# Optimization experiments

Measured on AMD Instinct MI355X. Metric: run time of the kernel, lower is better.

The kernel has to match this reference:

```python
import jax, jax.numpy as jnp
import numpy as np

T, IN, OUT = 16384, 4096, 4096


def setup_inputs() -> dict:
    key = jax.random.key(0)
    k1, k2, k3, k4, k5 = jax.random.split(key, 5)
    x = jax.random.randint(k1, (T, IN), -128, 128, dtype=jnp.int32)      # int8-valued activations
    weight = jax.random.randint(k2, (OUT, IN), -128, 128, dtype=jnp.int32)  # int8-valued weights
    bias = jax.random.randint(k3, (OUT,), -128, 128, dtype=jnp.int32)    # int8-valued bias
    # requant scales: alpha = a_scale*w_scale/o_scale, beta = b_scale/o_scale
    alpha = jax.random.uniform(k4, (1,), jnp.float32, 1e-4, 1e-3)
    beta = jax.random.uniform(k5, (1,), jnp.float32, 0.5, 1.5)
    return {"x": x, "weight": weight, "bias": bias, "alpha": alpha, "beta": beta}


def reference(x, weight, bias, alpha, beta):
    # INT8 GEMM with int32 accumulation: acc[t,o] = sum_i x[t,i] * W[o,i]
    acc = jnp.einsum('ti,oi->to', x, weight,
                     preferred_element_type=jnp.int32)  # [T, OUT] int32
    # inline dequant + bias + requant epilogue
    y = acc.astype(jnp.float32) * alpha + bias.astype(jnp.float32) * beta
    # round and saturate to int8 output (W8A8B8O8)
    out = jnp.clip(jnp.round(y), -128.0, 127.0).astype(jnp.int8)
    return out
```

## Files before the change

kernel.cpp:

```cpp
#include <hip/hip_runtime.h>
#include <stdint.h>

constexpr int T_DIM   = 16384;
constexpr int IN_DIM  = 4096;
constexpr int OUT_DIM = 4096;

using int32x4 = __attribute__((ext_vector_type(4))) int;

#define GLOAD_LDS16(g, l)                                                     \
    __builtin_amdgcn_global_load_lds(                                         \
        (const __attribute__((address_space(1))) void*)(uintptr_t)(g),        \
        (__attribute__((address_space(3))) void*)(uintptr_t)(l), 16, 0, 0)

__global__ void pack_swz(const int* __restrict__ src, int8_t* __restrict__ dst,
                         int rows, int cols) {
    int64_t tid = (int64_t)blockIdx.x * blockDim.x + threadIdx.x;
    int64_t nchunks = (int64_t)rows * (cols / 16);
    if (tid >= nchunks) return;
    int row  = (int)(tid / (cols / 16));
    int cidx = (int)(tid % (cols / 16));
    const int32x4* s4 =
        reinterpret_cast<const int32x4*>(src + (int64_t)row * cols + (cidx << 4));
    uint32_t p[4];
#pragma unroll
    for (int v = 0; v < 4; ++v) {
        int32x4 t = s4[v];
        p[v] = (uint32_t)(t[0] & 0xff) | ((uint32_t)(t[1] & 0xff) << 8) |
               ((uint32_t)(t[2] & 0xff) << 16) | ((uint32_t)(t[3] & 0xff) << 24);
    }
    int cs = (cidx & ~3) | ((cidx & 3) ^ ((row >> 1) & 3));
    *reinterpret_cast<int32x4*>(dst + (int64_t)row * cols + (cs << 4)) =
        *reinterpret_cast<int32x4*>(p);
}

constexpr int BM = 256, BN = 256, BK = 64;
constexpr int NT    = IN_DIM / BK;
constexpr int ATILE = BM * BK;
constexpr int BUFSZ = 2 * ATILE;

__global__ __launch_bounds__(512, 2)
void gemm_i8_8p(const int8_t* __restrict__ x8, const int8_t* __restrict__ w8,
                const int* __restrict__ bias, const float* __restrict__ alphap,
                const float* __restrict__ betap, int* __restrict__ out) {
    __shared__ __align__(16) int8_t lds[4 * BUFSZ];

    const int tid  = threadIdx.x;
    const int lane = tid & 63;
    const int wid  = tid >> 6;
    const int wr   = wid >> 2;
    const int wc   = wid & 3;

    const int nwg = gridDim.x;
    const int cpx = nwg >> 3;
    const int bid = blockIdx.x;
    const int swz = (bid & 7) * cpx + (bid >> 3);
    const int bm  = swz >> 4;
    const int bn  = swz & 15;
    const int brow = bm * BM;
    const int bcol = bn * BN;

    const float alpha = *alphap;
    const float beta  = *betap;

    const int g = lane >> 4;
    const int r = lane & 15;

    auto stageA = [&](int kt, int8_t* buf) {
#pragma unroll
        for (int l = 0; l < 2; ++l) {
            const int off = l * 8192 + tid * 16;
            const int row = off >> 6;
            GLOAD_LDS16(x8 + (int64_t)(brow + row) * IN_DIM + kt * BK + (off & 63),
                        buf + off);
        }
    };
    auto stageB = [&](int kt, int8_t* buf) {
#pragma unroll
        for (int l = 0; l < 2; ++l) {
            const int off = l * 8192 + tid * 16;
            const int row = off >> 6;
            GLOAD_LDS16(w8 + (int64_t)(bcol + row) * IN_DIM + kt * BK + (off & 63),
                        buf + ATILE + off);
        }
    };
    auto ldA = [&](const int8_t* Ab, int m) -> int32x4 {
        const int row = wr * 128 + m * 16 + r;
        const int sc  = g ^ ((row >> 1) & 3);
        return *reinterpret_cast<const int32x4*>(Ab + row * BK + (sc << 4));
    };
    auto ldB = [&](const int8_t* Bb, int n) -> int32x4 {
        const int row = wc * 64 + n * 16 + r;
        const int sc  = g ^ ((row >> 1) & 3);
        return *reinterpret_cast<const int32x4*>(Bb + row * BK + (sc << 4));
    };

    int32x4 acc[8][4] = {};

#define KTILE(T, BIDX, PF, VM)                                                 \
    do {                                                                       \
        const int8_t* Ab = lds + (BIDX) * BUFSZ;                               \
        const int8_t* Bb = Ab + ATILE;                                         \
        int8_t* nxt = lds + (((BIDX) + 3) & 3) * BUFSZ;                        \
        int32x4 bf[4], af[4];                                                  \
        _Pragma("unroll") for (int n = 0; n < 4; ++n) bf[n] = ldB(Bb, n);      \
        _Pragma("unroll") for (int m = 0; m < 4; ++m) af[m] = ldA(Ab, m);      \
        if (PF) stageA((T) + 3, nxt);                                          \
        __builtin_amdgcn_s_barrier();                                          \
        asm volatile("s_waitcnt lgkmcnt(0)");                                  \
        __builtin_amdgcn_s_setprio(1);                                         \
        _Pragma("unroll") for (int m = 0; m < 4; ++m)                          \
            _Pragma("unroll") for (int n = 0; n < 4; ++n)                      \
                acc[m][n] = __builtin_amdgcn_mfma_i32_16x16x64_i8(             \
                    af[m], bf[n], acc[m][n], 0, 0, 0);                         \
        __builtin_amdgcn_s_setprio(0);                                         \
        __builtin_amdgcn_s_barrier();                                          \
        _Pragma("unroll") for (int m = 0; m < 4; ++m) af[m] = ldA(Ab, 4 + m);  \
        if (PF) stageB((T) + 3, nxt);                                          \
        __builtin_amdgcn_s_barrier();                                          \
        asm volatile("s_waitcnt lgkmcnt(0)");                                  \
        __builtin_amdgcn_s_setprio(1);                                         \
        _Pragma("unroll") for (int m = 0; m < 4; ++m)                          \
            _Pragma("unroll") for (int n = 0; n < 4; ++n)                      \
                acc[4 + m][n] = __builtin_amdgcn_mfma_i32_16x16x64_i8(         \
                    af[m], bf[n], acc[4 + m][n], 0, 0, 0);                     \
        __builtin_amdgcn_s_setprio(0);                                         \
        if ((VM) == 8)      asm volatile("s_waitcnt vmcnt(8)" ::: "memory");   \
        else if ((VM) == 4) asm volatile("s_waitcnt vmcnt(4)" ::: "memory");   \
        else if ((VM) == 0) asm volatile("s_waitcnt vmcnt(0)" ::: "memory");   \
        __builtin_amdgcn_s_barrier();                                          \
        asm volatile("" ::: "memory");     \
    } while (0)

    stageA(0, lds);            stageB(0, lds);
    stageA(1, lds + BUFSZ);    stageB(1, lds + BUFSZ);
    stageA(2, lds + 2*BUFSZ);  stageB(2, lds + 2*BUFSZ);
    asm volatile("s_waitcnt vmcnt(8)" ::: "memory");
    __builtin_amdgcn_s_barrier();
    asm volatile("" ::: "memory");

#pragma unroll 1
    for (int tt = 0; tt < NT - 4; tt += 4) {
        KTILE(tt + 0, 0, true, 8);
        KTILE(tt + 1, 1, true, 8);
        KTILE(tt + 2, 2, true, 8);
        KTILE(tt + 3, 3, true, 8);
    }
    KTILE(NT - 4, 0, true,  8);
    KTILE(NT - 3, 1, false, 4);
    KTILE(NT - 2, 2, false, 0);
    KTILE(NT - 1, 3, false, -1);
#undef KTILE

    const int r4 = (lane >> 4) * 4;
    const int cl = lane & 15;
#pragma unroll
    for (int n = 0; n < 4; ++n) {
        const int col = bcol + wc * 64 + n * 16 + cl;
        const float bterm = (float)bias[col] * beta;
#pragma unroll
        for (int m = 0; m < 8; ++m) {
            const int row0 = brow + wr * 128 + m * 16 + r4;
#pragma unroll
            for (int j = 0; j < 4; ++j) {
                float y = (float)acc[m][n][j] * alpha + bterm;
                y = rintf(y);
                y = fminf(fmaxf(y, -128.0f), 127.0f);
                out[(int64_t)(row0 + j) * OUT_DIM + col] = (int)y;
            }
        }
    }
}

__global__ __launch_bounds__(256)
void gemm_i8_fb(const int* __restrict__ x32, const int* __restrict__ w32,
                const int* __restrict__ bias, const float* __restrict__ alphap,
                const float* __restrict__ betap, int* __restrict__ out) {
    constexpr int FBM = 128, FBK = 128;
    __shared__ int8_t lA[FBM * FBK];
    __shared__ int8_t lB[FBM * FBK];

    const int tid  = threadIdx.x;
    const int wid  = tid >> 6;
    const int lane = tid & 63;
    const int nwg = gridDim.x;
    const int cpx = nwg >> 3;
    const int bid = blockIdx.x;
    const int swz = (bid & 7) * cpx + (bid >> 3);
    const int brow = (swz >> 5) * FBM;
    const int bcol = (swz & 31) * FBM;
    const int wr = wid >> 1, wc = wid & 1;
    const float alpha = *alphap;
    const float beta  = *betap;

    int32x4 acc[4][4] = {};
    for (int kt = 0; kt < IN_DIM / FBK; ++kt) {
        const int64_t kbase = (int64_t)kt * FBK;
#pragma unroll
        for (int q = 0; q < 4; ++q) {
            const int off = wid * 4096 + q * 1024 + lane * 16;
            const int row = off >> 7;
            const int k   = off & 127;
            const int* ga = x32 + (int64_t)(brow + row) * IN_DIM + kbase + k;
            const int* gb = w32 + (int64_t)(bcol + row) * IN_DIM + kbase + k;
            uint32_t pa[4], pb[4];
#pragma unroll
            for (int v = 0; v < 4; ++v) {
                int32x4 ta = reinterpret_cast<const int32x4*>(ga)[v];
                int32x4 tb = reinterpret_cast<const int32x4*>(gb)[v];
                pa[v] = (uint32_t)(ta[0] & 0xff) | ((uint32_t)(ta[1] & 0xff) << 8) |
                        ((uint32_t)(ta[2] & 0xff) << 16) | ((uint32_t)(ta[3] & 0xff) << 24);
                pb[v] = (uint32_t)(tb[0] & 0xff) | ((uint32_t)(tb[1] & 0xff) << 8) |
                        ((uint32_t)(tb[2] & 0xff) << 16) | ((uint32_t)(tb[3] & 0xff) << 24);
            }
            const int sc = ((k >> 4) ^ (row & 7)) << 4;
            *reinterpret_cast<int32x4*>(lA + row * FBK + sc) = *reinterpret_cast<int32x4*>(pa);
            *reinterpret_cast<int32x4*>(lB + row * FBK + sc) = *reinterpret_cast<int32x4*>(pb);
        }
        __syncthreads();
#pragma unroll
        for (int ks = 0; ks < 2; ++ks) {
            const int gg = lane >> 4, rr = lane & 15;
            const int lc = ks * 4 + gg;
            int32x4 af[4], bf[4];
#pragma unroll
            for (int m = 0; m < 4; ++m) {
                const int row = wr * 64 + m * 16 + rr;
                af[m] = *reinterpret_cast<const int32x4*>(lA + row * FBK + ((lc ^ (row & 7)) << 4));
            }
#pragma unroll
            for (int n = 0; n < 4; ++n) {
                const int row = wc * 64 + n * 16 + rr;
                bf[n] = *reinterpret_cast<const int32x4*>(lB + row * FBK + ((lc ^ (row & 7)) << 4));
            }
#pragma unroll
            for (int m = 0; m < 4; ++m)
#pragma unroll
                for (int n = 0; n < 4; ++n)
                    acc[m][n] = __builtin_amdgcn_mfma_i32_16x16x64_i8(af[m], bf[n], acc[m][n], 0, 0, 0);
        }
        __syncthreads();
    }
    const int r4 = (lane >> 4) * 4;
    const int cl = lane & 15;
#pragma unroll
    for (int n = 0; n < 4; ++n) {
        const int col = bcol + wc * 64 + n * 16 + cl;
        const float bterm = (float)bias[col] * beta;
#pragma unroll
        for (int m = 0; m < 4; ++m) {
            const int row0 = brow + wr * 64 + m * 16 + r4;
#pragma unroll
            for (int j = 0; j < 4; ++j) {
                float y = (float)acc[m][n][j] * alpha + bterm;
                y = rintf(y);
                y = fminf(fmaxf(y, -128.0f), 127.0f);
                out[(int64_t)(row0 + j) * OUT_DIM + col] = (int)y;
            }
        }
    }
}

extern "C" void kernel_launch(void* const* d_in, const int* in_sizes, int n_in,
                              void* d_out, int out_size, void* d_ws, size_t ws_size,
                              hipStream_t stream) {
    const int*   x     = (const int*)d_in[0];
    const int*   w     = (const int*)d_in[1];
    const int*   bias  = (const int*)d_in[2];
    const float* alpha = (const float*)d_in[3];
    const float* beta  = (const float*)d_in[4];
    int*         out   = (int*)d_out;

    const size_t need = (size_t)T_DIM * IN_DIM + (size_t)OUT_DIM * IN_DIM;

    if (ws_size >= need) {
        int8_t* x8 = (int8_t*)d_ws;
        int8_t* w8 = x8 + (size_t)T_DIM * IN_DIM;
        {
            int64_t nch = (int64_t)T_DIM * (IN_DIM / 16);
            pack_swz<<<(int)((nch + 255) / 256), 256, 0, stream>>>(x, x8, T_DIM, IN_DIM);
        }
        {
            int64_t nch = (int64_t)OUT_DIM * (IN_DIM / 16);
            pack_swz<<<(int)((nch + 255) / 256), 256, 0, stream>>>(w, w8, OUT_DIM, IN_DIM);
        }
        const int grid = (T_DIM / BM) * (OUT_DIM / BN);
        gemm_i8_8p<<<grid, 512, 0, stream>>>(x8, w8, bias, alpha, beta, out);
    } else {
        const int grid = (T_DIM / 128) * (OUT_DIM / 128);
        gemm_i8_fb<<<grid, 256, 0, stream>>>(x, w, bias, alpha, beta, out);
    }
}
```

Measured before the change: 395.7 us.

## Collapse K-tile into single MFMA phase with precomputed LDS and global offsets

Restructures each K-tile step so all four global-to-LDS prefetches for the next stage are issued up front. All 8 A and 4 B fragments are then read from LDS and all 32 MFMAs run in one block, replacing the earlier two-phase split that needed three barriers per tile. Global pointers advance by BK each tile and LDS fragment offsets are precomputed once, which cuts per-tile address arithmetic. This is meant to reduce barrier and sync overhead, but holding all 8 A fragments raises VGPR pressure and removes the interleaving of LDS reads with MFMA.

After: 394.6 us. Within noise of the previous version (-0.3%).

```diff
diff --git a/kernel.cpp b/kernel.cpp
--- a/kernel.cpp
+++ b/kernel.cpp
@@ -65,90 +65,80 @@
     const int g = lane >> 4;
     const int r = lane & 15;
 
-    auto stageA = [&](int kt, int8_t* buf) {
-#pragma unroll
-        for (int l = 0; l < 2; ++l) {
-            const int off = l * 8192 + tid * 16;
-            const int row = off >> 6;
-            GLOAD_LDS16(x8 + (int64_t)(brow + row) * IN_DIM + kt * BK + (off & 63),
-                        buf + off);
-        }
-    };
-    auto stageB = [&](int kt, int8_t* buf) {
-#pragma unroll
-        for (int l = 0; l < 2; ++l) {
-            const int off = l * 8192 + tid * 16;
-            const int row = off >> 6;
-            GLOAD_LDS16(w8 + (int64_t)(bcol + row) * IN_DIM + kt * BK + (off & 63),
-                        buf + ATILE + off);
-        }
-    };
-    auto ldA = [&](const int8_t* Ab, int m) -> int32x4 {
+    const int offL0 = tid * 16;
+    const int offL1 = 8192 + tid * 16;
+    const int rowL0 = offL0 >> 6, inL0 = offL0 & 63;
+    const int rowL1 = offL1 >> 6, inL1 = offL1 & 63;
+    const int8_t* pA0 = x8 + (int64_t)(brow + rowL0) * IN_DIM + inL0;
+    const int8_t* pA1 = x8 + (int64_t)(brow + rowL1) * IN_DIM + inL1;
+    const int8_t* pB0 = w8 + (int64_t)(bcol + rowL0) * IN_DIM + inL0;
+    const int8_t* pB1 = w8 + (int64_t)(bcol + rowL1) * IN_DIM + inL1;
+    const int dA0 = offL0, dA1 = offL1;
+    const int dB0 = ATILE + offL0, dB1 = ATILE + offL1;
+
+    int aoff[8], boff[4];
+#pragma unroll
+    for (int m = 0; m < 8; ++m) {
         const int row = wr * 128 + m * 16 + r;
-        const int sc  = g ^ ((row >> 1) & 3);
-        return *reinterpret_cast<const int32x4*>(Ab + row * BK + (sc << 4));
-    };
-    auto ldB = [&](const int8_t* Bb, int n) -> int32x4 {
+        aoff[m] = row * BK + ((g ^ ((row >> 1) & 3)) << 4);
+    }
+#pragma unroll
+    for (int n = 0; n < 4; ++n) {
         const int row = wc * 64 + n * 16 + r;
-        const int sc  = g ^ ((row >> 1) & 3);
-        return *reinterpret_cast<const int32x4*>(Bb + row * BK + (sc << 4));
-    };
+        boff[n] = ATILE + row * BK + ((g ^ ((row >> 1) & 3)) << 4);
+    }
 
     int32x4 acc[8][4] = {};
 
-#define KTILE(T, BIDX, PF, VM)                                                 \
+#define KTILE(BIDX, PF, VM)                                                    \
     do {                                                                       \
-        const int8_t* Ab = lds + (BIDX) * BUFSZ;                               \
-        const int8_t* Bb = Ab + ATILE;                                         \
+        const int8_t* buf = lds + (BIDX) * BUFSZ;                              \
         int8_t* nxt = lds + (((BIDX) + 3) & 3) * BUFSZ;                        \
-        int32x4 bf[4], af[4];                                                  \
-        _Pragma("unroll") for (int n = 0; n < 4; ++n) bf[n] = ldB(Bb, n);      \
-        _Pragma("unroll") for (int m = 0; m < 4; ++m) af[m] = ldA(Ab, m);      \
-        if (PF) stageA((T) + 3, nxt);                                          \
-        __builtin_amdgcn_s_barrier();                                          \
-        asm volatile("s_waitcnt lgkmcnt(0)");                                  \
+        if (PF) {                                                              \
+            GLOAD_LDS16(pA0, nxt + dA0);  GLOAD_LDS16(pA1, nxt + dA1);         \
+            GLOAD_LDS16(pB0, nxt + dB0);  GLOAD_LDS16(pB1, nxt + dB1);         \
+            pA0 += BK; pA1 += BK; pB0 += BK; pB1 += BK;                        \
+        }                                                                      \
+        int32x4 af[8], bf[4];                                                  \
+        _Pragma("unroll") for (int n = 0; n < 4; ++n)                          \
+            bf[n] = *reinterpret_cast<const int32x4*>(buf + boff[n]);          \
+        _Pragma("unroll") for (int m = 0; m < 8; ++m)                          \
+            af[m] = *reinterpret_cast<const int32x4*>(buf + aoff[m]);          \
         __builtin_amdgcn_s_setprio(1);                                         \
-        _Pragma("unroll") for (int m = 0; m < 4; ++m)                          \
+        _Pragma("unroll") for (int m = 0; m < 8; ++m)                          \
             _Pragma("unroll") for (int n = 0; n < 4; ++n)                      \
                 acc[m][n] = __builtin_amdgcn_mfma_i32_16x16x64_i8(             \
                     af[m], bf[n], acc[m][n], 0, 0, 0);                         \
-        __builtin_amdgcn_s_setprio(0);                                         \
-        __builtin_amdgcn_s_barrier();                                          \
-        _Pragma("unroll") for (int m = 0; m < 4; ++m) af[m] = ldA(Ab, 4 + m);  \
-        if (PF) stageB((T) + 3, nxt);                                          \
-        __builtin_amdgcn_s_barrier();                                          \
-        asm volatile("s_waitcnt lgkmcnt(0)");                                  \
-        __builtin_amdgcn_s_setprio(1);                                         \
-        _Pragma("unroll") for (int m = 0; m < 4; ++m)                          \
-            _Pragma("unroll") for (int n = 0; n < 4; ++n)                      \
-                acc[4 + m][n] = __builtin_amdgcn_mfma_i32_16x16x64_i8(         \
-                    af[m], bf[n], acc[4 + m][n], 0, 0, 0);                     \
         __builtin_amdgcn_s_setprio(0);                                         \
         if ((VM) == 8)      asm volatile("s_waitcnt vmcnt(8)" ::: "memory");   \
         else if ((VM) == 4) asm volatile("s_waitcnt vmcnt(4)" ::: "memory");   \
         else if ((VM) == 0) asm volatile("s_waitcnt vmcnt(0)" ::: "memory");   \
         __builtin_amdgcn_s_barrier();                                          \
-        asm volatile("" ::: "memory");     \
+        asm volatile("" ::: "memory");       \
     } while (0)
 
-    stageA(0, lds);            stageB(0, lds);
-    stageA(1, lds + BUFSZ);    stageB(1, lds + BUFSZ);
-    stageA(2, lds + 2*BUFSZ);  stageB(2, lds + 2*BUFSZ);
+#pragma unroll
+    for (int t = 0; t < 3; ++t) {
+        int8_t* buf = lds + t * BUFSZ;
+        GLOAD_LDS16(pA0, buf + dA0);  GLOAD_LDS16(pA1, buf + dA1);
+        GLOAD_LDS16(pB0, buf + dB0);  GLOAD_LDS16(pB1, buf + dB1);
+        pA0 += BK; pA1 += BK; pB0 += BK; pB1 += BK;
+    }
     asm volatile("s_waitcnt vmcnt(8)" ::: "memory");
     __builtin_amdgcn_s_barrier();
     asm volatile("" ::: "memory");
 
 #pragma unroll 1
     for (int tt = 0; tt < NT - 4; tt += 4) {
-        KTILE(tt + 0, 0, true, 8);
-        KTILE(tt + 1, 1, true, 8);
-        KTILE(tt + 2, 2, true, 8);
-        KTILE(tt + 3, 3, true, 8);
-    }
-    KTILE(NT - 4, 0, true,  8);
-    KTILE(NT - 3, 1, false, 4);
-    KTILE(NT - 2, 2, false, 0);
-    KTILE(NT - 1, 3, false, -1);
+        KTILE(0, true, 8);
+        KTILE(1, true, 8);
+        KTILE(2, true, 8);
+        KTILE(3, true, 8);
+    }
+    KTILE(0, true,  8);
+    KTILE(1, false, 4);
+    KTILE(2, false, 0);
+    KTILE(3, false, -1);
 #undef KTILE
 
     const int r4 = (lane >> 4) * 4;
```
